# Kernel optimization log

Hardware: AMD Instinct MI355X
Metric: run time of the kernel (lower is better)

## Reference

```python
import jax, jax.numpy as jnp
import numpy as np

SQRT_D = 8.0

def setup_inputs() -> dict:
    key = jax.random.key(0)
    kq, kk, kv = jax.random.split(key, 3)
    shape = (2, 16, 2048, 64)  # [batch, heads, seq, head_dim]
    return {
        "q": jax.random.normal(kq, shape, dtype=jnp.float32),
        "k": jax.random.normal(kk, shape, dtype=jnp.float32),
        "v": jax.random.normal(kv, shape, dtype=jnp.float32),
    }

def reference(q, k, v):
    # score = softmax(QK^T / sqrt_d) over the key axis j
    scores = jnp.einsum('bhif,bhjf->bhij', q, k) / SQRT_D
    probs = jax.nn.softmax(scores, axis=-1)
    # Note: original returns output permuted to [b, i, h, f]
    attn = jnp.einsum('bhij,bhjf->bihf', probs, v)
    return attn
```

## Files before the change

kernel.cpp:

```cpp
#include <hip/hip_runtime.h>

#define S_LEN 2048
#define HEADS 16
#define DIM 64

typedef __attribute__((ext_vector_type(8))) short short8;
typedef __attribute__((ext_vector_type(16))) float float16v;
typedef __attribute__((ext_vector_type(4))) float float4v;
typedef __attribute__((ext_vector_type(4))) unsigned uint4v;

static __device__ __forceinline__ unsigned pkbf(float lo, float hi) {
  unsigned r;
  asm("v_cvt_pk_bf16_f32 %0, %1, %2" : "=v"(r) : "v"(lo), "v"(hi));
  return r;
}

static __device__ __forceinline__ void gll16(const short* g, short* l) {
  __builtin_amdgcn_global_load_lds(
      (const __attribute__((address_space(1))) void*)g,
      (__attribute__((address_space(3))) void*)l, 16, 0, 0);
}

__global__ __launch_bounds__(256) void prep(const float* __restrict__ kk,
                                            const float* __restrict__ vv,
                                            short* __restrict__ kb,
                                            short* __restrict__ vt) {
  __shared__ unsigned t32[64 * 33];
  const int bx = blockIdx.x;
  const int bh = bx >> 5;
  const int j0 = (bx & 31) * 64;
  const int tid = threadIdx.x;

  {
    const int j = tid >> 2, f0 = (tid & 3) * 16;
    const float4v* src = (const float4v*)(kk + ((size_t)bh * S_LEN + j0 + j) * DIM + f0);
    float4v a0 = src[0], a1 = src[1], a2 = src[2], a3 = src[3];
    uint4v w0, w1;
    w0[0] = pkbf(a0[0], a0[1]); w0[1] = pkbf(a0[2], a0[3]);
    w0[2] = pkbf(a1[0], a1[1]); w0[3] = pkbf(a1[2], a1[3]);
    w1[0] = pkbf(a2[0], a2[1]); w1[1] = pkbf(a2[2], a2[3]);
    w1[2] = pkbf(a3[0], a3[1]); w1[3] = pkbf(a3[2], a3[3]);
    uint4v* dst = (uint4v*)(kb + ((size_t)bh * S_LEN + j0 + j) * DIM + f0);
    dst[0] = w0; dst[1] = w1;
  }
  {
    const int jp = (tid & 31) * 2, f0 = (tid >> 5) * 8;
    const int pp = ((jp & ~12) | ((jp & 4) << 1) | ((jp & 8) >> 1)) >> 1;
    const float* r0 = vv + ((size_t)bh * S_LEN + j0 + jp) * DIM + f0;
    const float* r1 = r0 + DIM;
    float4v a0 = *(const float4v*)r0, a1 = *(const float4v*)(r0 + 4);
    float4v b0 = *(const float4v*)r1, b1 = *(const float4v*)(r1 + 4);
#pragma unroll
    for (int e = 0; e < 4; e++) {
      t32[(f0 + e) * 33 + pp]     = pkbf(a0[e], b0[e]);
      t32[(f0 + 4 + e) * 33 + pp] = pkbf(a1[e], b1[e]);
    }
  }
  __syncthreads();
  {
    const int f = tid >> 2, x0 = (tid & 3) * 8;
    uint4v c0 = *(const uint4v*)&t32[f * 33 + x0];
    uint4v c1 = *(const uint4v*)&t32[f * 33 + x0 + 4];
    uint4v* dst = (uint4v*)(vt + ((size_t)bh * DIM + f) * S_LEN + j0 + x0 * 2);
    dst[0] = c0; dst[1] = c1;
  }
}

__global__ __launch_bounds__(128, 2) void attn_fwd(const float* __restrict__ q,
                                                   const short* __restrict__ kb,
                                                   const short* __restrict__ vt,
                                                   float* __restrict__ out) {
  __shared__ alignas(16) float smem[64 * 68];
  short* const k_lds = (short*)smem;
  short* const v_lds = k_lds + 4096;

  const int bx = blockIdx.x;
  const int bh = bx >> 5, it = bx & 31;
  const int b = bh >> 4, h = bh & 15;
  const int tid = threadIdx.x;
  const int w = tid >> 6, lane = tid & 63;
  const int n = lane & 31, hf = lane >> 5;
  const int i0 = it * 64 + w * 32;

  short8 qa[4];
  {
    const float* qrow = q + ((size_t)bh * S_LEN + i0 + n) * DIM + hf * 8;
#pragma unroll
    for (int ks = 0; ks < 4; ks++) {
      float4v x0 = *(const float4v*)(qrow + ks * 16);
      float4v x1 = *(const float4v*)(qrow + ks * 16 + 4);
      uint4v pk_;
      pk_[0] = pkbf(x0[0] * 0.125f, x0[1] * 0.125f);
      pk_[1] = pkbf(x0[2] * 0.125f, x0[3] * 0.125f);
      pk_[2] = pkbf(x1[0] * 0.125f, x1[1] * 0.125f);
      pk_[3] = pkbf(x1[2] * 0.125f, x1[3] * 0.125f);
      qa[ks] = *(short8*)&pk_;
    }
  }

  float16v acc0, acc1;
#pragma unroll
  for (int e = 0; e < 16; e++) { acc0[e] = 0.f; acc1[e] = 0.f; }
  float lp = 0.f;

  const short* kbase = kb + (size_t)bh * S_LEN * DIM;
  const short* vbase = vt + (size_t)bh * DIM * S_LEN;

  for (int j0 = 0; j0 < S_LEN; j0 += 64) {
    __syncthreads();
#pragma unroll
    for (int qi = 0; qi < 4; qi++) {
      const int ib = w * 4 + qi;
      const int jl = ib * 8 + (lane >> 3);
      const int ch = (lane & 7) ^ (jl & 7);
      gll16(kbase + (size_t)(j0 + jl) * DIM + ch * 8, &k_lds[ib * 512]);
      gll16(vbase + (size_t)jl * S_LEN + j0 + ch * 8, &v_lds[ib * 512]);
    }
    __syncthreads();

    float16v st0, st1;
#pragma unroll
    for (int e = 0; e < 16; e++) { st0[e] = 0.f; st1[e] = 0.f; }
#pragma unroll
    for (int ks = 0; ks < 4; ks++) {
      const int cpos = (2 * ks + hf) ^ (n & 7);
      short8 kf0 = *(const short8*)&k_lds[(n * 8 + cpos) * 8];
      short8 kf1 = *(const short8*)&k_lds[((32 + n) * 8 + cpos) * 8];
      st0 = __builtin_amdgcn_mfma_f32_32x32x16_bf16(kf0, qa[ks], st0, 0, 0, 0);
      st1 = __builtin_amdgcn_mfma_f32_32x32x16_bf16(kf1, qa[ks], st1, 0, 0, 0);
    }

#pragma unroll
    for (int e = 0; e < 16; e++) {
      st0[e] = __expf(st0[e]);
      st1[e] = __expf(st1[e]);
      lp += st0[e] + st1[e];
    }

    uint4v pb[4];
#pragma unroll
    for (int u = 0; u < 4; u++) {
      pb[0][u] = pkbf(st0[2 * u], st0[2 * u + 1]);
      pb[1][u] = pkbf(st0[8 + 2 * u], st0[8 + 2 * u + 1]);
      pb[2][u] = pkbf(st1[2 * u], st1[2 * u + 1]);
      pb[3][u] = pkbf(st1[8 + 2 * u], st1[8 + 2 * u + 1]);
    }

#pragma unroll
    for (int c = 0; c < 4; c++) {
      const int cpos = (2 * c + hf) ^ (n & 7);
      short8 vf0 = *(const short8*)&v_lds[(n * 8 + cpos) * 8];
      short8 vf1 = *(const short8*)&v_lds[((32 + n) * 8 + cpos) * 8];
      short8 pa = *(short8*)&pb[c];
      acc0 = __builtin_amdgcn_mfma_f32_32x32x16_bf16(vf0, pa, acc0, 0, 0, 0);
      acc1 = __builtin_amdgcn_mfma_f32_32x32x16_bf16(vf1, pa, acc1, 0, 0, 0);
    }
  }

  const float tot = lp + __shfl_xor(lp, 32);
  const float inv = 1.f / tot;

  __syncthreads();
  float* const ob = smem;
#pragma unroll
  for (int a = 0; a < 4; a++) {
    float4v t0, t1;
#pragma unroll
    for (int e = 0; e < 4; e++) {
      t0[e] = acc0[4 * a + e] * inv;
      t1[e] = acc1[4 * a + e] * inv;
    }
    const int row = w * 32 + n;
    *(float4v*)&ob[row * 68 + 8 * a + 4 * hf] = t0;
    *(float4v*)&ob[row * 68 + 32 + 8 * a + 4 * hf] = t1;
  }
  __syncthreads();
  {
    const int il = tid >> 1, fq = (tid & 1) * 32;
    const float* src = &ob[il * 68 + fq];
    float* dst = out + (((size_t)b * S_LEN + it * 64 + il) * HEADS + h) * DIM + fq;
#pragma unroll
    for (int u = 0; u < 8; u++) ((float4v*)dst)[u] = ((const float4v*)src)[u];
  }
}

extern "C" void kernel_launch(void* const* d_in, const int* in_sizes, int n_in,
                              void* d_out, int out_size, void* d_ws, size_t ws_size,
                              hipStream_t stream) {
  const float* q = (const float*)d_in[0];
  const float* k = (const float*)d_in[1];
  const float* v = (const float*)d_in[2];
  float* out = (float*)d_out;
  short* kb = (short*)d_ws;
  short* vt = (short*)d_ws + (size_t)32 * S_LEN * DIM;

  prep<<<1024, 256, 0, stream>>>(k, v, kb, vt);
  attn_fwd<<<1024, 128, 0, stream>>>(q, kb, vt, out);
}
```

Measured before the change: 145.5 us.

## Process two query sub-tiles per wave to double K/V reuse per load

Each wave now handles 64 query rows instead of 32, so every K/V fragment read from LDS feeds four MFMAs instead of two, and each block covers 128 rows. This halves the grid to 512 blocks and halves global K/V tile traffic per query row. In exchange it doubles accumulator and score register pressure, lowers launch_bounds occupancy to 1, and leaves fewer blocks to spread across CUs.

Result: no change. 147.3 us (+1.2%).

```diff
diff --git a/kernel.cpp b/kernel.cpp
--- a/kernel.cpp
+++ b/kernel.cpp
@@ -30,7 +30,6 @@
   const int bh = bx >> 5;
   const int j0 = (bx & 31) * 64;
   const int tid = threadIdx.x;
-
   {
     const int j = tid >> 2, f0 = (tid & 3) * 16;
     const float4v* src = (const float4v*)(kk + ((size_t)bh * S_LEN + j0 + j) * DIM + f0);
@@ -66,25 +65,26 @@
   }
 }
 
-__global__ __launch_bounds__(128, 2) void attn_fwd(const float* __restrict__ q,
+__global__ __launch_bounds__(128, 1) void attn_fwd(const float* __restrict__ q,
                                                    const short* __restrict__ kb,
                                                    const short* __restrict__ vt,
                                                    float* __restrict__ out) {
-  __shared__ alignas(16) float smem[64 * 68];
+  __shared__ alignas(16) float smem[128 * 68];
   short* const k_lds = (short*)smem;
   short* const v_lds = k_lds + 4096;
 
   const int bx = blockIdx.x;
-  const int bh = bx >> 5, it = bx & 31;
+  const int bh = bx >> 4, it = bx & 15;
   const int b = bh >> 4, h = bh & 15;
   const int tid = threadIdx.x;
   const int w = tid >> 6, lane = tid & 63;
   const int n = lane & 31, hf = lane >> 5;
-  const int i0 = it * 64 + w * 32;
-
-  short8 qa[4];
-  {
-    const float* qrow = q + ((size_t)bh * S_LEN + i0 + n) * DIM + hf * 8;
+  const int i0 = it * 128 + w * 64;
+
+  short8 qa[2][4];
+#pragma unroll
+  for (int s = 0; s < 2; s++) {
+    const float* qrow = q + ((size_t)bh * S_LEN + i0 + s * 32 + n) * DIM + hf * 8;
 #pragma unroll
     for (int ks = 0; ks < 4; ks++) {
       float4v x0 = *(const float4v*)(qrow + ks * 16);
@@ -94,14 +94,14 @@
       pk_[1] = pkbf(x0[2] * 0.125f, x0[3] * 0.125f);
       pk_[2] = pkbf(x1[0] * 0.125f, x1[1] * 0.125f);
       pk_[3] = pkbf(x1[2] * 0.125f, x1[3] * 0.125f);
-      qa[ks] = *(short8*)&pk_;
-    }
-  }
-
-  float16v acc0, acc1;
-#pragma unroll
-  for (int e = 0; e < 16; e++) { acc0[e] = 0.f; acc1[e] = 0.f; }
-  float lp = 0.f;
+      qa[s][ks] = *(short8*)&pk_;
+    }
+  }
+
+  float16v acc00, acc01, acc10, acc11;
+#pragma unroll
+  for (int e = 0; e < 16; e++) { acc00[e] = 0.f; acc01[e] = 0.f; acc10[e] = 0.f; acc11[e] = 0.f; }
+  float lp0 = 0.f, lp1 = 0.f;
 
   const short* kbase = kb + (size_t)bh * S_LEN * DIM;
   const short* vbase = vt + (size_t)bh * DIM * S_LEN;
@@ -118,32 +118,32 @@
     }
     __syncthreads();
 
-    float16v st0, st1;
-#pragma unroll
-    for (int e = 0; e < 16; e++) { st0[e] = 0.f; st1[e] = 0.f; }
+    float16v st00, st01, st10, st11;
+#pragma unroll
+    for (int e = 0; e < 16; e++) { st00[e] = 0.f; st01[e] = 0.f; st10[e] = 0.f; st11[e] = 0.f; }
 #pragma unroll
     for (int ks = 0; ks < 4; ks++) {
       const int cpos = (2 * ks + hf) ^ (n & 7);
       short8 kf0 = *(const short8*)&k_lds[(n * 8 + cpos) * 8];
       short8 kf1 = *(const short8*)&k_lds[((32 + n) * 8 + cpos) * 8];
-      st0 = __builtin_amdgcn_mfma_f32_32x32x16_bf16(kf0, qa[ks], st0, 0, 0, 0);
-      st1 = __builtin_amdgcn_mfma_f32_32x32x16_bf16(kf1, qa[ks], st1, 0, 0, 0);
-    }
-
-#pragma unroll
-    for (int e = 0; e < 16; e++) {
-      st0[e] = __expf(st0[e]);
-      st1[e] = __expf(st1[e]);
-      lp += st0[e] + st1[e];
-    }
-
-    uint4v pb[4];
+      st00 = __builtin_amdgcn_mfma_f32_32x32x16_bf16(kf0, qa[0][ks], st00, 0, 0, 0);
+      st01 = __builtin_amdgcn_mfma_f32_32x32x16_bf16(kf1, qa[0][ks], st01, 0, 0, 0);
+      st10 = __builtin_amdgcn_mfma_f32_32x32x16_bf16(kf0, qa[1][ks], st10, 0, 0, 0);
+      st11 = __builtin_amdgcn_mfma_f32_32x32x16_bf16(kf1, qa[1][ks], st11, 0, 0, 0);
+    }
+
+    uint4v pb0[4], pb1[4];
 #pragma unroll
     for (int u = 0; u < 4; u++) {
-      pb[0][u] = pkbf(st0[2 * u], st0[2 * u + 1]);
-      pb[1][u] = pkbf(st0[8 + 2 * u], st0[8 + 2 * u + 1]);
-      pb[2][u] = pkbf(st1[2 * u], st1[2 * u + 1]);
-      pb[3][u] = pkbf(st1[8 + 2 * u], st1[8 + 2 * u + 1]);
+      float e0, e1;
+      e0 = __expf(st00[2 * u]);     e1 = __expf(st00[2 * u + 1]);     lp0 += e0 + e1; pb0[0][u] = pkbf(e0, e1);
+      e0 = __expf(st00[8 + 2 * u]); e1 = __expf(st00[8 + 2 * u + 1]); lp0 += e0 + e1; pb0[1][u] = pkbf(e0, e1);
+      e0 = __expf(st01[2 * u]);     e1 = __expf(st01[2 * u + 1]);     lp0 += e0 + e1; pb0[2][u] = pkbf(e0, e1);
+      e0 = __expf(st01[8 + 2 * u]); e1 = __expf(st01[8 + 2 * u + 1]); lp0 += e0 + e1; pb0[3][u] = pkbf(e0, e1);
+      e0 = __expf(st10[2 * u]);     e1 = __expf(st10[2 * u + 1]);     lp1 += e0 + e1; pb1[0][u] = pkbf(e0, e1);
+      e0 = __expf(st10[8 + 2 * u]); e1 = __expf(st10[8 + 2 * u + 1]); lp1 += e0 + e1; pb1[1][u] = pkbf(e0, e1);
+      e0 = __expf(st11[2 * u]);     e1 = __expf(st11[2 * u + 1]);     lp1 += e0 + e1; pb1[2][u] = pkbf(e0, e1);
+      e0 = __expf(st11[8 + 2 * u]); e1 = __expf(st11[8 + 2 * u + 1]); lp1 += e0 + e1; pb1[3][u] = pkbf(e0, e1);
     }
 
 #pragma unroll
@@ -151,34 +151,37 @@
       const int cpos = (2 * c + hf) ^ (n & 7);
       short8 vf0 = *(const short8*)&v_lds[(n * 8 + cpos) * 8];
       short8 vf1 = *(const short8*)&v_lds[((32 + n) * 8 + cpos) * 8];
-      short8 pa = *(short8*)&pb[c];
-      acc0 = __builtin_amdgcn_mfma_f32_32x32x16_bf16(vf0, pa, acc0, 0, 0, 0);
-      acc1 = __builtin_amdgcn_mfma_f32_32x32x16_bf16(vf1, pa, acc1, 0, 0, 0);
-    }
-  }
-
-  const float tot = lp + __shfl_xor(lp, 32);
-  const float inv = 1.f / tot;
+      acc00 = __builtin_amdgcn_mfma_f32_32x32x16_bf16(vf0, *(short8*)&pb0[c], acc00, 0, 0, 0);
+      acc01 = __builtin_amdgcn_mfma_f32_32x32x16_bf16(vf1, *(short8*)&pb0[c], acc01, 0, 0, 0);
+      acc10 = __builtin_amdgcn_mfma_f32_32x32x16_bf16(vf0, *(short8*)&pb1[c], acc10, 0, 0, 0);
+      acc11 = __builtin_amdgcn_mfma_f32_32x32x16_bf16(vf1, *(short8*)&pb1[c], acc11, 0, 0, 0);
+    }
+  }
+
+  const float inv0 = 1.f / (lp0 + __shfl_xor(lp0, 32));
+  const float inv1 = 1.f / (lp1 + __shfl_xor(lp1, 32));
 
   __syncthreads();
-  float* const ob = smem;
 #pragma unroll
   for (int a = 0; a < 4; a++) {
-    float4v t0, t1;
+    float4v t00, t01, t10, t11;
 #pragma unroll
     for (int e = 0; e < 4; e++) {
-      t0[e] = acc0[4 * a + e] * inv;
-      t1[e] = acc1[4 * a + e] * inv;
-    }
-    const int row = w * 32 + n;
-    *(float4v*)&ob[row * 68 + 8 * a + 4 * hf] = t0;
-    *(float4v*)&ob[row * 68 + 32 + 8 * a + 4 * hf] = t1;
+      t00[e] = acc00[4 * a + e] * inv0; t01[e] = acc01[4 * a + e] * inv0;
+      t10[e] = acc10[4 * a + e] * inv1; t11[e] = acc11[4 * a + e] * inv1;
+    }
+    const int fo = 8 * a + 4 * hf;
+    *(float4v*)&smem[(w * 64 + n) * 68 + fo]           = t00;
+    *(float4v*)&smem[(w * 64 + n) * 68 + 32 + fo]      = t01;
+    *(float4v*)&smem[(w * 64 + 32 + n) * 68 + fo]      = t10;
+    *(float4v*)&smem[(w * 64 + 32 + n) * 68 + 32 + fo] = t11;
   }
   __syncthreads();
-  {
-    const int il = tid >> 1, fq = (tid & 1) * 32;
-    const float* src = &ob[il * 68 + fq];
-    float* dst = out + (((size_t)b * S_LEN + it * 64 + il) * HEADS + h) * DIM + fq;
+#pragma unroll
+  for (int r2 = 0; r2 < 2; r2++) {
+    const int il = r2 * 64 + (tid >> 1), fq = (tid & 1) * 32;
+    const float* src = &smem[il * 68 + fq];
+    float* dst = out + (((size_t)b * S_LEN + it * 128 + il) * HEADS + h) * DIM + fq;
 #pragma unroll
     for (int u = 0; u < 8; u++) ((float4v*)dst)[u] = ((const float4v*)src)[u];
   }
@@ -195,5 +198,5 @@
   short* vt = (short*)d_ws + (size_t)32 * S_LEN * DIM;
 
   prep<<<1024, 256, 0, stream>>>(k, v, kb, vt);
-  attn_fwd<<<1024, 128, 0, stream>>>(q, kb, vt, out);
-}
+  attn_fwd<<<512, 128, 0, stream>>>(q, kb, vt, out);
+}
```
